# Kernel tuning notes

Hardware: AMD Instinct MI355X
Metric: run time of the kernel (lower is better)

The kernel has to match this reference:

```python
import jax, jax.numpy as jnp
import numpy as np

N = 100000   # nodes
E = 600000   # edges
D = 128      # d_model
R = 200      # num_relations


def setup_inputs() -> dict:
    key = jax.random.key(0)
    ks = jax.random.split(key, 12)
    def nrm(k, shape, scale=0.02):
        return jax.random.normal(k, shape, jnp.float32) * scale
    return dict(
        node_features=jax.random.normal(ks[0], (N, D), jnp.float32),
        edge_index=jax.random.randint(ks[1], (2, E), 0, N),
        edge_type=jax.random.randint(ks[2], (E,), 0, R),
        rel_embed=nrm(ks[3], (R, D)),
        msg_w1=nrm(ks[4], (2 * D, D)), msg_b1=jnp.zeros((D,), jnp.float32),
        msg_w2=nrm(ks[5], (D, D)), msg_b2=jnp.zeros((D,), jnp.float32),
        attn_w1=nrm(ks[6], (2 * D, D)), attn_b1=jnp.zeros((D,), jnp.float32),
        attn_w2=nrm(ks[7], (D, 1)), attn_b2=jnp.zeros((1,), jnp.float32),
        ln1_g=jnp.ones((D,), jnp.float32), ln1_b=jnp.zeros((D,), jnp.float32),
        ffn_w1=nrm(ks[8], (D, 4 * D)), ffn_b1=jnp.zeros((4 * D,), jnp.float32),
        ffn_w2=nrm(ks[9], (4 * D, D)), ffn_b2=jnp.zeros((D,), jnp.float32),
        ln2_g=jnp.ones((D,), jnp.float32), ln2_b=jnp.zeros((D,), jnp.float32),
    )


def layer_norm(x, g, b, eps=1e-5):
    mu = x.mean(-1, keepdims=True)
    var = ((x - mu) ** 2).mean(-1, keepdims=True)
    return (x - mu) * jax.lax.rsqrt(var + eps) * g + b


def reference(node_features, edge_index, edge_type, rel_embed,
              msg_w1, msg_b1, msg_w2, msg_b2,
              attn_w1, attn_b1, attn_w2, attn_b2,
              ln1_g, ln1_b, ffn_w1, ffn_b1, ffn_w2, ffn_b2,
              ln2_g, ln2_b):
    Nn = node_features.shape[0]
    src, dst = edge_index[0], edge_index[1]
    # gather + edge message MLP
    src_feat = node_features[src]              # [E, D]
    rel_feat = rel_embed[edge_type]            # [E, D]
    h = jnp.concatenate([src_feat, rel_feat], axis=-1)          # [E, 2D]
    messages = jax.nn.relu(h @ msg_w1 + msg_b1) @ msg_w2 + msg_b2  # [E, D]
    # edge attention logits
    a_in = jnp.concatenate([node_features[dst], messages], axis=-1)  # [E, 2D]
    attn_raw = (jax.nn.leaky_relu(a_in @ attn_w1 + attn_b1, 0.2) @ attn_w2 + attn_b2)[:, 0]  # [E]
    # two-pass segment softmax over destination nodes
    attn_max = jax.ops.segment_max(attn_raw, dst, num_segments=Nn)   # [N]
    attn_exp = jnp.exp(attn_raw - attn_max[dst])                      # [E]
    attn_sum = jax.ops.segment_sum(attn_exp, dst, num_segments=Nn)   # [N]
    attn_w = attn_exp / (attn_sum[dst] + 1e-8)                        # [E]
    # scatter-add weighted messages
    aggr = jax.ops.segment_sum(attn_w[:, None] * messages, dst, num_segments=Nn)  # [N, D]
    x = layer_norm(node_features + aggr, ln1_g, ln1_b)
    ffn = jax.nn.gelu(x @ ffn_w1 + ffn_b1, approximate=False) @ ffn_w2 + ffn_b2
    return layer_norm(x + ffn, ln2_g, ln2_b)
```

## Files before the change

kernel.cpp:

```cpp
#include <hip/hip_runtime.h>
#include <hip/hip_bf16.h>

#define NN 100000
#define NE 600000
#define DD 128
#define RR 200
#define SCAN_NB ((NN + 255) / 256)

typedef __attribute__((ext_vector_type(8))) short bf16x8;
typedef __attribute__((ext_vector_type(4))) float f32x4;

__device__ __forceinline__ unsigned int bfbits(float x) {
    return (unsigned int)__builtin_bit_cast(unsigned short, __float2bfloat16(x));
}
__device__ __forceinline__ unsigned int pk2(float a, float b) {
    return bfbits(a) | (bfbits(b) << 16);
}
__device__ __forceinline__ unsigned short bf16s(float x) {
    return __builtin_bit_cast(unsigned short, __float2bfloat16(x));
}
__device__ __forceinline__ float unbf(unsigned short u) {
    return __builtin_bit_cast(float, ((unsigned int)u) << 16);
}
__device__ __forceinline__ float unlo(unsigned int u) {
    return __builtin_bit_cast(float, u << 16);
}
__device__ __forceinline__ float unhi(unsigned int u) {
    return __builtin_bit_cast(float, u & 0xffff0000u);
}

__device__ __forceinline__ void gload_lds16(const void* g, void* l) {
    __builtin_amdgcn_global_load_lds(
        (const __attribute__((address_space(1))) void*)g,
        (__attribute__((address_space(3))) void*)l, 16, 0, 0);
}

__global__ void k_initc(int* __restrict__ cnt) {
    int i = blockIdx.x * 256 + threadIdx.x;
    if (i < NN) cnt[i] = 0;
}

__global__ void k_hist(const int* __restrict__ dst, int* __restrict__ cnt) {
    int e = blockIdx.x * 256 + threadIdx.x;
    if (e < NE) atomicAdd(&cnt[dst[e]], 1);
}

__global__ void k_scanA(const int* __restrict__ cnt, int* __restrict__ bsum) {
    __shared__ int red[256];
    int i = blockIdx.x * 256 + threadIdx.x;
    red[threadIdx.x] = (i < NN) ? cnt[i] : 0;
    __syncthreads();
    for (int off = 128; off >= 1; off >>= 1) {
        if (threadIdx.x < off) red[threadIdx.x] += red[threadIdx.x + off];
        __syncthreads();
    }
    if (threadIdx.x == 0) bsum[blockIdx.x] = red[0];
}

__global__ void k_scanB(int* __restrict__ bsum) {
    __shared__ int sh[512];
    int t = threadIdx.x;
    int v = (t < SCAN_NB) ? bsum[t] : 0;
    sh[t] = v;
    __syncthreads();
    for (int off = 1; off < 512; off <<= 1) {
        int add = (t >= off) ? sh[t - off] : 0;
        __syncthreads();
        sh[t] += add;
        __syncthreads();
    }
    if (t < SCAN_NB) bsum[t] = sh[t] - v;
}

__global__ void k_scanC(const int* __restrict__ cnt, const int* __restrict__ bsum,
                        int* __restrict__ row_start, int* __restrict__ cursor) {
    __shared__ int sh[256];
    int i = blockIdx.x * 256 + threadIdx.x;
    int t = threadIdx.x;
    int v = (i < NN) ? cnt[i] : 0;
    sh[t] = v;
    __syncthreads();
    for (int off = 1; off < 256; off <<= 1) {
        int add = (t >= off) ? sh[t - off] : 0;
        __syncthreads();
        sh[t] += add;
        __syncthreads();
    }
    if (i < NN) {
        int ex = bsum[blockIdx.x] + sh[t] - v;
        row_start[i] = ex;
        cursor[i] = ex;
    }
}

__global__ void k_bucket(const int* __restrict__ dst, int* __restrict__ cursor,
                         int* __restrict__ eid) {
    int e = blockIdx.x * 256 + threadIdx.x;
    if (e < NE) {
        int p = atomicAdd(&cursor[dst[e]], 1);
        eid[p] = e;
    }
}

__global__ void k_prep(const float* __restrict__ nf, unsigned short* __restrict__ nfb) {
    int i = blockIdx.x * 256 + threadIdx.x;
    if (i >= NN * DD / 8) return;
    const float* sp = nf + (size_t)i * 8;
    float4 f0 = *reinterpret_cast<const float4*>(sp);
    float4 f1 = *reinterpret_cast<const float4*>(sp + 4);
    uint4 v;
    v.x = pk2(f0.x, f0.y); v.y = pk2(f0.z, f0.w);
    v.z = pk2(f1.x, f1.y); v.w = pk2(f1.z, f1.w);
    *reinterpret_cast<uint4*>(nfb + (size_t)i * 8) = v;
}

__global__ void k_relc(const float* __restrict__ rel, const float* __restrict__ mw1,
                       const float* __restrict__ mb1, unsigned short* __restrict__ relcb) {
    int idx = blockIdx.x * 256 + threadIdx.x;
    if (idx >= RR * DD) return;
    int r = idx >> 7, n = idx & 127;
    float s = mb1[n];
    for (int k = 0; k < 128; ++k)
        s = fmaf(rel[r * 128 + k], mw1[(128 + k) * 128 + n], s);
    relcb[idx] = bf16s(s);
}

__global__ void k_mwb(const float* __restrict__ mw2, const float* __restrict__ mb2,
                      const float* __restrict__ aw1,
                      float* __restrict__ mwB, float* __restrict__ zb) {
    int idx = blockIdx.x * 256 + threadIdx.x;
    if (idx < 16384) {
        int k = idx >> 7, n = idx & 127;
        float s = 0.0f;
        for (int j = 0; j < 128; ++j)
            s = fmaf(mw2[k * 128 + j], aw1[(128 + j) * 128 + n], s);
        mwB[idx] = s;
    } else if (idx < 16512) {
        int n = idx - 16384;
        float s = 0.0f;
        for (int j = 0; j < 128; ++j)
            s = fmaf(mb2[j], aw1[(128 + j) * 128 + n], s);
        zb[n] = s;
    }
}

__global__ void k_pack(const float* __restrict__ mw1, const float* __restrict__ mw2,
                       const float* __restrict__ mwB,
                       const float* __restrict__ aw1,
                       const float* __restrict__ fw1, const float* __restrict__ fw2,
                       unsigned short* __restrict__ mw1p,
                       unsigned short* __restrict__ mwCp,
                       unsigned short* __restrict__ awTp,
                       unsigned short* __restrict__ fw1p,
                       unsigned short* __restrict__ fw2p) {
    int idx = blockIdx.x * 256 + threadIdx.x;
    if (idx < 16384) {
        int i = idx & 7, l = (idx >> 3) & 63, ks = (idx >> 9) & 3, nt = idx >> 11;
        int k = ks * 32 + (l >> 4) * 8 + i, n = nt * 16 + (l & 15);
        mw1p[idx] = bf16s(mw1[k * 128 + n]);
    } else if (idx < 49152) {
        int j = idx - 16384;
        int i = j & 7, l = (j >> 3) & 63, ks = (j >> 9) & 3, nt = j >> 11;
        int k = ks * 32 + (l >> 4) * 8 + i, n = nt * 16 + (l & 15);
        mwCp[j] = bf16s((n < 128) ? mw2[k * 128 + n] : mwB[k * 128 + (n - 128)]);
    } else if (idx < 65536) {
        int j = idx - 49152;
        int i = j & 7, l = (j >> 3) & 63, ks = (j >> 9) & 3, nt = j >> 11;
        int k = ks * 32 + (l >> 4) * 8 + i, n = nt * 16 + (l & 15);
        awTp[j] = bf16s(aw1[k * 128 + n]);
    } else if (idx < 131072) {
        int j = idx - 65536;
        int i = j & 7, l = (j >> 3) & 63, ks = (j >> 9) & 3, nt = j >> 11;
        int k = ks * 32 + (l >> 4) * 8 + i, n = nt * 16 + (l & 15);
        fw1p[j] = bf16s(fw1[k * 512 + n]);
    } else if (idx < 196608) {
        int j = idx - 131072;
        int i = j & 7, l = (j >> 3) & 63, ks = (j >> 9) & 15, nt = j >> 13;
        int k = ks * 32 + (l >> 4) * 8 + i, n = nt * 16 + (l & 15);
        fw2p[j] = bf16s(fw2[k * 128 + n]);
    }
}

__global__ __launch_bounds__(256) void k_nfa(
    const unsigned short* __restrict__ nfb, const unsigned short* __restrict__ awTp,
    const float* __restrict__ ab1, unsigned short* __restrict__ nfa)
{
    __shared__ alignas(16) unsigned short XB[64 * 128];
    const int t = threadIdx.x;
    const int w = t >> 6, l = t & 63;
    const int wm = w >> 1, wn = w & 1;
    const int lm = l & 15, lk = l >> 4;
    const int lrow = l >> 4, lslot = l & 15;
    const int n0 = blockIdx.x * 64;

    #pragma unroll
    for (int it = 0; it < 4; ++it) {
        int rb = w * 16 + it * 4;
        int row = rb + lrow;
        long grow = n0 + row; if (grow >= NN) grow = NN - 1;
        int c = lslot ^ (row & 7);
        gload_lds16(nfb + grow * DD + c * 8, &XB[rb * 128]);
    }
    __syncthreads();

    f32x4 acc[2][4];
    #pragma unroll
    for (int mf = 0; mf < 2; ++mf)
        #pragma unroll
        for (int nfr = 0; nfr < 4; ++nfr) acc[mf][nfr] = (f32x4){0.f, 0.f, 0.f, 0.f};

    #pragma unroll
    for (int ks = 0; ks < 4; ++ks) {
        bf16x8 a[2];
        #pragma unroll
        for (int mf = 0; mf < 2; ++mf) {
            int m = wm * 32 + mf * 16 + lm;
            int slot = (ks * 4 + lk) ^ (m & 7);
            a[mf] = *reinterpret_cast<const bf16x8*>(&XB[m * 128 + slot * 8]);
        }
        #pragma unroll
        for (int nfr = 0; nfr < 4; ++nfr) {
            int nt = wn * 4 + nfr;
            bf16x8 b = *reinterpret_cast<const bf16x8*>(&awTp[((nt * 4 + ks) * 64 + l) * 8]);
            acc[0][nfr] = __builtin_amdgcn_mfma_f32_16x16x32_bf16(a[0], b, acc[0][nfr], 0, 0, 0);
            acc[1][nfr] = __builtin_amdgcn_mfma_f32_16x16x32_bf16(a[1], b, acc[1][nfr], 0, 0, 0);
        }
    }
    __syncthreads();

    #pragma unroll
    for (int nfr = 0; nfr < 4; ++nfr) {
        int n = wn * 64 + nfr * 16 + lm;
        float bv = ab1[n];
        #pragma unroll
        for (int mf = 0; mf < 2; ++mf)
            #pragma unroll
            for (int r = 0; r < 4; ++r) {
                int m = wm * 32 + mf * 16 + lk * 4 + r;
                XB[m * 128 + n] = bf16s(acc[mf][nfr][r] + bv);
            }
    }
    __syncthreads();

    #pragma unroll
    for (int j = 0; j < 4; ++j) {
        int q = j * 256 + t;
        int row = q >> 4, c16 = q & 15;
        if (n0 + row < NN)
            *reinterpret_cast<uint4*>(&nfa[(size_t)(n0 + row) * DD + c16 * 8]) =
                *reinterpret_cast<const uint4*>(&XB[row * 128 + c16 * 8]);
    }
}

__global__ __launch_bounds__(512) void k_edge(
    const unsigned short* __restrict__ nfb, const int* __restrict__ src,
    const int* __restrict__ dst, const int* __restrict__ etype,
    const unsigned short* __restrict__ nfa, const unsigned short* __restrict__ relcb,
    const unsigned short* __restrict__ mw1p, const unsigned short* __restrict__ mwCp,
    const float* __restrict__ mb2, const float* __restrict__ zb,
    const float* __restrict__ aw2, const float* __restrict__ ab2,
    unsigned short* __restrict__ msg_out, float* __restrict__ attn_raw)
{
    __shared__ alignas(16) unsigned short S[64 * 128];
    __shared__ alignas(16) unsigned short H[64 * 128];
    __shared__ alignas(16) unsigned short MS[64 * 128];
    __shared__ float RED[64][2];

    const int t = threadIdx.x;
    const int w = t >> 6, l = t & 63;
    const int wm = w >> 2, wn = w & 3;
    const int lm = l & 15, lk = l >> 4;
    const int lrow = l >> 4, lslot = l & 15;
    const int e0 = blockIdx.x * 64;

    #pragma unroll
    for (int it = 0; it < 2; ++it) {
        int rb = w * 8 + it * 4;
        int row = rb + lrow;
        int c = lslot ^ (row & 7);
        gload_lds16(nfb + (size_t)src[e0 + row] * DD + c * 8, &S[rb * 128]);
    }
    #pragma unroll
    for (int it = 0; it < 2; ++it) {
        int rb = w * 8 + it * 4;
        int row = rb + lrow;
        int c = lslot ^ (row & 7);
        gload_lds16(relcb + (size_t)etype[e0 + row] * DD + c * 8, &MS[rb * 128]);
    }
    __syncthreads();

    {
        f32x4 acc[2][2];
        #pragma unroll
        for (int mf = 0; mf < 2; ++mf)
            #pragma unroll
            for (int nfr = 0; nfr < 2; ++nfr) acc[mf][nfr] = (f32x4){0.f, 0.f, 0.f, 0.f};

        #pragma unroll
        for (int ks = 0; ks < 4; ++ks) {
            bf16x8 a[2];
            #pragma unroll
            for (int mf = 0; mf < 2; ++mf) {
                int m = wm * 32 + mf * 16 + lm;
                int slot = (ks * 4 + lk) ^ (m & 7);
                a[mf] = *reinterpret_cast<const bf16x8*>(&S[m * 128 + slot * 8]);
            }
            #pragma unroll
            for (int nfr = 0; nfr < 2; ++nfr) {
                int nt = wn * 2 + nfr;
                bf16x8 b = *reinterpret_cast<const bf16x8*>(&mw1p[((nt * 4 + ks) * 64 + l) * 8]);
                acc[0][nfr] = __builtin_amdgcn_mfma_f32_16x16x32_bf16(a[0], b, acc[0][nfr], 0, 0, 0);
                acc[1][nfr] = __builtin_amdgcn_mfma_f32_16x16x32_bf16(a[1], b, acc[1][nfr], 0, 0, 0);
            }
        }
        #pragma unroll
        for (int nfr = 0; nfr < 2; ++nfr) {
            int n = (wn * 2 + nfr) * 16 + lm;
            #pragma unroll
            for (int mf = 0; mf < 2; ++mf)
                #pragma unroll
                for (int r = 0; r < 4; ++r) {
                    int m = wm * 32 + mf * 16 + lk * 4 + r;
                    float v = acc[mf][nfr][r] + unbf(MS[m * 128 + ((n >> 3) ^ (m & 7)) * 8 + (n & 7)]);
                    v = fmaxf(v, 0.0f);
                    H[m * 128 + ((n >> 3) ^ (m & 7)) * 8 + (n & 7)] = bf16s(v);
                }
        }
    }
    __syncthreads();

    #pragma unroll
    for (int it = 0; it < 2; ++it) {
        int rb = w * 8 + it * 4;
        int row = rb + lrow;
        int c = lslot ^ (row & 7);
        gload_lds16(nfa + (size_t)dst[e0 + row] * DD + c * 8, &S[rb * 128]);
    }

    f32x4 acc[2][4];
    #pragma unroll
    for (int mf = 0; mf < 2; ++mf)
        #pragma unroll
        for (int nfr = 0; nfr < 4; ++nfr) acc[mf][nfr] = (f32x4){0.f, 0.f, 0.f, 0.f};

    #pragma unroll
    for (int ks = 0; ks < 4; ++ks) {
        bf16x8 a[2];
        #pragma unroll
        for (int mf = 0; mf < 2; ++mf) {
            int m = wm * 32 + mf * 16 + lm;
            int slot = (ks * 4 + lk) ^ (m & 7);
            a[mf] = *reinterpret_cast<const bf16x8*>(&H[m * 128 + slot * 8]);
        }
        #pragma unroll
        for (int nfr = 0; nfr < 4; ++nfr) {
            int nt = wn * 4 + nfr;
            bf16x8 b = *reinterpret_cast<const bf16x8*>(&mwCp[((nt * 4 + ks) * 64 + l) * 8]);
            acc[0][nfr] = __builtin_amdgcn_mfma_f32_16x16x32_bf16(a[0], b, acc[0][nfr], 0, 0, 0);
            acc[1][nfr] = __builtin_amdgcn_mfma_f32_16x16x32_bf16(a[1], b, acc[1][nfr], 0, 0, 0);
        }
    }
    __syncthreads();

    if (wn < 2) {
        #pragma unroll
        for (int nfr = 0; nfr < 4; ++nfr) {
            int n = (wn * 4 + nfr) * 16 + lm;
            float bv = mb2[n];
            #pragma unroll
            for (int mf = 0; mf < 2; ++mf)
                #pragma unroll
                for (int r = 0; r < 4; ++r) {
                    int m = wm * 32 + mf * 16 + lk * 4 + r;
                    MS[m * 128 + ((n >> 3) ^ (m & 7)) * 8 + (n & 7)] = bf16s(acc[mf][nfr][r] + bv);
                }
        }
    } else {
        float zbv[4], aw2v[4];
        #pragma unroll
        for (int nfr = 0; nfr < 4; ++nfr) {
            int nc = (wn - 2) * 64 + nfr * 16 + lm;
            zbv[nfr] = zb[nc];
            aw2v[nfr] = aw2[nc];
        }
        #pragma unroll
        for (int mf = 0; mf < 2; ++mf)
            #pragma unroll
            for (int r = 0; r < 4; ++r) {
                int m = wm * 32 + mf * 16 + lk * 4 + r;
                float s = 0.0f;
                #pragma unroll
                for (int nfr = 0; nfr < 4; ++nfr) {
                    int nc = (wn - 2) * 64 + nfr * 16 + lm;
                    float v = acc[mf][nfr][r] + zbv[nfr]
                            + unbf(S[m * 128 + ((nc >> 3) ^ (m & 7)) * 8 + (nc & 7)]);
                    v = (v > 0.0f) ? v : 0.2f * v;
                    s = fmaf(v, aw2v[nfr], s);
                }
                s += __shfl_xor(s, 1, 64);
                s += __shfl_xor(s, 2, 64);
                s += __shfl_xor(s, 4, 64);
                s += __shfl_xor(s, 8, 64);
                if (lm == 0) RED[m][wn - 2] = s;
            }
    }
    __syncthreads();

    #pragma unroll
    for (int j = 0; j < 2; ++j) {
        int q = j * 512 + t;
        int row = q >> 4, c16 = q & 15;
        int slot = c16 ^ (row & 7);
        *reinterpret_cast<uint4*>(&msg_out[(size_t)(e0 + row) * DD + c16 * 8]) =
            *reinterpret_cast<const uint4*>(&MS[row * 128 + slot * 8]);
    }
    if (t < 64) {
        attn_raw[e0 + t] = RED[t][0] + RED[t][1] + ab2[0];
    }
}

__global__ __launch_bounds__(256) void k_aggr(
    const unsigned short* __restrict__ msg, const float* __restrict__ raw,
    const int* __restrict__ row_start, const int* __restrict__ cnt,
    const int* __restrict__ eid, float* __restrict__ aggr)
{
    const int l = threadIdx.x & 63;
    const int n = blockIdx.x * 4 + (threadIdx.x >> 6);
    if (n >= NN) return;
    const int rs = row_start[n], deg = cnt[n];

    float m = -INFINITY;
    for (int j = l; j < deg; j += 64) m = fmaxf(m, raw[eid[rs + j]]);
    #pragma unroll
    for (int off = 32; off >= 1; off >>= 1) m = fmaxf(m, __shfl_xor(m, off, 64));

    float s = 0.0f;
    for (int j = l; j < deg; j += 64) s += expf(raw[eid[rs + j]] - m);
    #pragma unroll
    for (int off = 32; off >= 1; off >>= 1) s += __shfl_xor(s, off, 64);
    const float rinv = 1.0f / (s + 1e-8f);

    float a0 = 0.0f, a1 = 0.0f;
    for (int base = 0; base < deg; base += 64) {
        int nt = min(64, deg - base);
        int e_l = 0; float w_l = 0.0f;
        if (l < nt) {
            e_l = eid[rs + base + l];
            w_l = expf(raw[e_l] - m) * rinv;
        }
        for (int j = 0; j < nt; ++j) {
            int e = __shfl(e_l, j, 64);
            float w = __shfl(w_l, j, 64);
            unsigned int v = *reinterpret_cast<const unsigned int*>(&msg[(size_t)e * DD + l * 2]);
            a0 = fmaf(w, unlo(v), a0);
            a1 = fmaf(w, unhi(v), a1);
        }
    }
    float2 o = {a0, a1};
    *reinterpret_cast<float2*>(&aggr[(size_t)n * DD + l * 2]) = o;
}

__global__ __launch_bounds__(512) void k_node(
    const float* __restrict__ nf, const float* __restrict__ aggr,
    const float* __restrict__ g1, const float* __restrict__ b1,
    const unsigned short* __restrict__ fw1p, const float* __restrict__ fb1,
    const unsigned short* __restrict__ fw2p, const float* __restrict__ fb2,
    const float* __restrict__ g2, const float* __restrict__ b2,
    float* __restrict__ out)
{
    __shared__ alignas(16) unsigned short XB[64 * 128];
    __shared__ alignas(16) unsigned short HB[64 * 256];

    const int t = threadIdx.x;
    const int w = t >> 6, l = t & 63;
    const int wm = w >> 2, wn = w & 3;
    const int lm = l & 15, lk = l >> 4;
    const int row = t >> 3;
    const int q = t & 7;
    const long n0 = (long)blockIdx.x * 64;
    const long rg = n0 + row;
    const long rc = (rg < NN) ? rg : (NN - 1);

    float xr[16];
    float s = 0.0f, ss = 0.0f;
    {
        const float* xp = nf + rc * DD + q * 16;
        const float* ap = aggr + rc * DD + q * 16;
        #pragma unroll
        for (int i = 0; i < 4; ++i) {
            float4 a = *reinterpret_cast<const float4*>(xp + i * 4);
            float4 b = *reinterpret_cast<const float4*>(ap + i * 4);
            float v0 = a.x + b.x, v1 = a.y + b.y, v2 = a.z + b.z, v3 = a.w + b.w;
            xr[i * 4 + 0] = v0; xr[i * 4 + 1] = v1; xr[i * 4 + 2] = v2; xr[i * 4 + 3] = v3;
            s += v0 + v1 + v2 + v3;
            ss = fmaf(v0, v0, ss); ss = fmaf(v1, v1, ss);
            ss = fmaf(v2, v2, ss); ss = fmaf(v3, v3, ss);
        }
    }
    s  += __shfl_xor(s, 1, 64);  s  += __shfl_xor(s, 2, 64);  s  += __shfl_xor(s, 4, 64);
    ss += __shfl_xor(ss, 1, 64); ss += __shfl_xor(ss, 2, 64); ss += __shfl_xor(ss, 4, 64);
    {
        float mu = s * (1.0f / DD);
        float var = ss * (1.0f / DD) - mu * mu;
        float rstd = rsqrtf(var + 1e-5f);
        #pragma unroll
        for (int i = 0; i < 4; ++i) {
            float4 gv = *reinterpret_cast<const float4*>(g1 + q * 16 + i * 4);
            float4 bv = *reinterpret_cast<const float4*>(b1 + q * 16 + i * 4);
            xr[i * 4 + 0] = (xr[i * 4 + 0] - mu) * rstd * gv.x + bv.x;
            xr[i * 4 + 1] = (xr[i * 4 + 1] - mu) * rstd * gv.y + bv.y;
            xr[i * 4 + 2] = (xr[i * 4 + 2] - mu) * rstd * gv.z + bv.z;
            xr[i * 4 + 3] = (xr[i * 4 + 3] - mu) * rstd * gv.w + bv.w;
        }
        #pragma unroll
        for (int i = 0; i < 2; ++i) {
            int c = q * 2 + i, slot = c ^ (row & 7);
            uint4 v;
            v.x = pk2(xr[i * 8 + 0], xr[i * 8 + 1]);
            v.y = pk2(xr[i * 8 + 2], xr[i * 8 + 3]);
            v.z = pk2(xr[i * 8 + 4], xr[i * 8 + 5]);
            v.w = pk2(xr[i * 8 + 6], xr[i * 8 + 7]);
            *reinterpret_cast<uint4*>(&XB[row * 128 + slot * 8]) = v;
        }
    }
    __syncthreads();

    f32x4 acc2[2][2];
    #pragma unroll
    for (int mf = 0; mf < 2; ++mf)
        #pragma unroll
        for (int nfr = 0; nfr < 2; ++nfr) acc2[mf][nfr] = (f32x4){0.f, 0.f, 0.f, 0.f};

    #pragma unroll
    for (int half = 0; half < 2; ++half) {
        f32x4 acc[2][4];
        #pragma unroll
        for (int mf = 0; mf < 2; ++mf)
            #pragma unroll
            for (int nfr = 0; nfr < 4; ++nfr) acc[mf][nfr] = (f32x4){0.f, 0.f, 0.f, 0.f};

        #pragma unroll
        for (int ks = 0; ks < 4; ++ks) {
            bf16x8 a[2];
            #pragma unroll
            for (int mf = 0; mf < 2; ++mf) {
                int m = wm * 32 + mf * 16 + lm;
                int slot = (ks * 4 + lk) ^ (m & 7);
                a[mf] = *reinterpret_cast<const bf16x8*>(&XB[m * 128 + slot * 8]);
            }
            #pragma unroll
            for (int nfr = 0; nfr < 4; ++nfr) {
                int nt = half * 16 + wn * 4 + nfr;
                bf16x8 b = *reinterpret_cast<const bf16x8*>(&fw1p[((nt * 4 + ks) * 64 + l) * 8]);
                acc[0][nfr] = __builtin_amdgcn_mfma_f32_16x16x32_bf16(a[0], b, acc[0][nfr], 0, 0, 0);
                acc[1][nfr] = __builtin_amdgcn_mfma_f32_16x16x32_bf16(a[1], b, acc[1][nfr], 0, 0, 0);
            }
        }
        #pragma unroll
        for (int nfr = 0; nfr < 4; ++nfr) {
            int nl = (wn * 4 + nfr) * 16 + lm;
            float bv = fb1[half * 256 + nl];
            #pragma unroll
            for (int mf = 0; mf < 2; ++mf)
                #pragma unroll
                for (int r = 0; r < 4; ++r) {
                    int m = wm * 32 + mf * 16 + lk * 4 + r;
                    float h = acc[mf][nfr][r] + bv;
                    float e = __expf(h * -1.702f);
                    float gvv = h * __builtin_amdgcn_rcpf(1.0f + e);
                    HB[m * 256 + (((nl >> 3) ^ (m & 7)) * 8) + (nl & 7)] = bf16s(gvv);
                }
        }
        __syncthreads();

        #pragma unroll
        for (int ks = 0; ks < 8; ++ks) {
            bf16x8 a[2];
            #pragma unroll
            for (int mf = 0; mf < 2; ++mf) {
                int m = wm * 32 + mf * 16 + lm;
                int slot = (ks * 4 + lk) ^ (m & 7);
                a[mf] = *reinterpret_cast<const bf16x8*>(&HB[m * 256 + slot * 8]);
            }
            #pragma unroll
            for (int nfr = 0; nfr < 2; ++nfr) {
                int nt = wn * 2 + nfr;
                int kg = half * 8 + ks;
                bf16x8 b = *reinterpret_cast<const bf16x8*>(&fw2p[((nt * 16 + kg) * 64 + l) * 8]);
                acc2[0][nfr] = __builtin_amdgcn_mfma_f32_16x16x32_bf16(a[0], b, acc2[0][nfr], 0, 0, 0);
                acc2[1][nfr] = __builtin_amdgcn_mfma_f32_16x16x32_bf16(a[1], b, acc2[1][nfr], 0, 0, 0);
            }
        }
        __syncthreads();
    }

    #pragma unroll
    for (int nfr = 0; nfr < 2; ++nfr) {
        int n = (wn * 2 + nfr) * 16 + lm;
        float bv = fb2[n];
        #pragma unroll
        for (int mf = 0; mf < 2; ++mf)
            #pragma unroll
            for (int r = 0; r < 4; ++r) {
                int m = wm * 32 + mf * 16 + lk * 4 + r;
                XB[m * 128 + (((n >> 3) ^ (m & 7)) * 8) + (n & 7)] = bf16s(acc2[mf][nfr][r] + bv);
            }
    }
    __syncthreads();

    float s2 = 0.0f, ss2 = 0.0f;
    #pragma unroll
    for (int i = 0; i < 2; ++i) {
        int c = q * 2 + i, slot = c ^ (row & 7);
        uint4 v = *reinterpret_cast<const uint4*>(&XB[row * 128 + slot * 8]);
        float f[8];
        f[0] = unlo(v.x); f[1] = unhi(v.x); f[2] = unlo(v.y); f[3] = unhi(v.y);
        f[4] = unlo(v.z); f[5] = unhi(v.z); f[6] = unlo(v.w); f[7] = unhi(v.w);
        #pragma unroll
        for (int j = 0; j < 8; ++j) {
            float vv = xr[i * 8 + j] + f[j];
            xr[i * 8 + j] = vv;
            s2 += vv;
            ss2 = fmaf(vv, vv, ss2);
        }
    }
    s2  += __shfl_xor(s2, 1, 64);  s2  += __shfl_xor(s2, 2, 64);  s2  += __shfl_xor(s2, 4, 64);
    ss2 += __shfl_xor(ss2, 1, 64); ss2 += __shfl_xor(ss2, 2, 64); ss2 += __shfl_xor(ss2, 4, 64);
    {
        float mu = s2 * (1.0f / DD);
        float var = ss2 * (1.0f / DD) - mu * mu;
        float rstd = rsqrtf(var + 1e-5f);
        if (rg < NN) {
            float* op = out + rg * DD + q * 16;
            #pragma unroll
            for (int i = 0; i < 4; ++i) {
                float4 gv = *reinterpret_cast<const float4*>(g2 + q * 16 + i * 4);
                float4 bv = *reinterpret_cast<const float4*>(b2 + q * 16 + i * 4);
                float4 o;
                o.x = (xr[i * 4 + 0] - mu) * rstd * gv.x + bv.x;
                o.y = (xr[i * 4 + 1] - mu) * rstd * gv.y + bv.y;
                o.z = (xr[i * 4 + 2] - mu) * rstd * gv.z + bv.z;
                o.w = (xr[i * 4 + 3] - mu) * rstd * gv.w + bv.w;
                *reinterpret_cast<float4*>(op + i * 4) = o;
            }
        }
    }
}

extern "C" void kernel_launch(void* const* d_in, const int* in_sizes, int n_in,
                              void* d_out, int out_size, void* d_ws, size_t ws_size,
                              hipStream_t stream)
{
    const float* nf  = (const float*)d_in[0];
    const int*   ei  = (const int*)d_in[1];
    const int*   et  = (const int*)d_in[2];
    const float* rel = (const float*)d_in[3];
    const float* mw1 = (const float*)d_in[4];
    const float* mb1 = (const float*)d_in[5];
    const float* mw2 = (const float*)d_in[6];
    const float* mb2 = (const float*)d_in[7];
    const float* aw1 = (const float*)d_in[8];
    const float* ab1 = (const float*)d_in[9];
    const float* aw2 = (const float*)d_in[10];
    const float* ab2 = (const float*)d_in[11];
    const float* g1  = (const float*)d_in[12];
    const float* b1  = (const float*)d_in[13];
    const float* fw1 = (const float*)d_in[14];
    const float* fb1 = (const float*)d_in[15];
    const float* fw2 = (const float*)d_in[16];
    const float* fb2 = (const float*)d_in[17];
    const float* g2  = (const float*)d_in[18];
    const float* b2  = (const float*)d_in[19];
    float* out = (float*)d_out;

    char* ws = (char*)d_ws;
    size_t off = 0;
    auto alloc = [&](size_t bytes) -> char* {
        char* p = ws + off;
        off += (bytes + 255) & ~(size_t)255;
        return p;
    };
    unsigned short* msg = (unsigned short*)alloc((size_t)NE * DD * 2);
    float* attn_raw = (float*)alloc((size_t)NE * 4);
    float* aggr     = (float*)alloc((size_t)NN * DD * 4);
    unsigned short* nfb  = (unsigned short*)alloc((size_t)NN * DD * 2);
    unsigned short* relcb = (unsigned short*)alloc((size_t)RR * DD * 2);
    float* mwB = (float*)alloc((size_t)16384 * 4);
    float* zb  = (float*)alloc((size_t)128 * 4);
    int* cnt       = (int*)alloc((size_t)NN * 4);
    int* row_start = (int*)alloc((size_t)NN * 4);
    int* cursor    = (int*)alloc((size_t)NN * 4);
    int* eid       = (int*)alloc((size_t)NE * 4);
    int* bsum      = (int*)alloc((size_t)SCAN_NB * 4);
    unsigned short* mw1p = (unsigned short*)alloc(16384 * 2);
    unsigned short* mwCp = (unsigned short*)alloc(32768 * 2);
    unsigned short* awTp = (unsigned short*)alloc(16384 * 2);
    unsigned short* fw1p = (unsigned short*)alloc(65536 * 2);
    unsigned short* fw2p = (unsigned short*)alloc(65536 * 2);

    unsigned short* nfa = (unsigned short*)aggr;

    const int* srcp = ei;
    const int* dstp = ei + NE;

    hipLaunchKernelGGL(k_initc, dim3(SCAN_NB), dim3(256), 0, stream, cnt);
    hipLaunchKernelGGL(k_hist, dim3((NE + 255) / 256), dim3(256), 0, stream, dstp, cnt);
    hipLaunchKernelGGL(k_scanA, dim3(SCAN_NB), dim3(256), 0, stream, cnt, bsum);
    hipLaunchKernelGGL(k_scanB, dim3(1), dim3(512), 0, stream, bsum);
    hipLaunchKernelGGL(k_scanC, dim3(SCAN_NB), dim3(256), 0, stream, cnt, bsum, row_start, cursor);
    hipLaunchKernelGGL(k_bucket, dim3((NE + 255) / 256), dim3(256), 0, stream, dstp, cursor, eid);
    hipLaunchKernelGGL(k_prep, dim3(NN * DD / 8 / 256), dim3(256), 0, stream, nf, nfb);
    hipLaunchKernelGGL(k_mwb, dim3(65), dim3(256), 0, stream, mw2, mb2, aw1, mwB, zb);
    hipLaunchKernelGGL(k_pack, dim3(768), dim3(256), 0, stream,
                       mw1, mw2, mwB, aw1, fw1, fw2, mw1p, mwCp, awTp, fw1p, fw2p);
    hipLaunchKernelGGL(k_relc, dim3(100), dim3(256), 0, stream, rel, mw1, mb1, relcb);
    hipLaunchKernelGGL(k_nfa, dim3((NN + 63) / 64), dim3(256), 0, stream,
                       nfb, awTp, ab1, nfa);
    hipLaunchKernelGGL(k_edge, dim3(NE / 64), dim3(512), 0, stream,
                       nfb, srcp, dstp, et, nfa, relcb,
                       mw1p, mwCp, mb2, zb, aw2, ab2,
                       msg, attn_raw);
    hipLaunchKernelGGL(k_aggr, dim3((NN + 3) / 4), dim3(256), 0, stream,
                       msg, attn_raw, row_start, cnt, eid, aggr);
    hipLaunchKernelGGL(k_node, dim3((NN + 63) / 64), dim3(512), 0, stream,
                       nf, aggr, g1, b1, fw1p, fb1, fw2p, fb2, g2, b2, out);
}
```

Measured before the change: 482.2 us.

## Process edges in destination-sorted order so aggregation reads contiguous messages

Result: faster. 471.6 us (-2.2%).

```diff
diff --git a/kernel.cpp b/kernel.cpp
--- a/kernel.cpp
+++ b/kernel.cpp
@@ -93,12 +93,17 @@
     }
 }
 
-__global__ void k_bucket(const int* __restrict__ dst, int* __restrict__ cursor,
-                         int* __restrict__ eid) {
+__global__ void k_bucket(const int* __restrict__ src, const int* __restrict__ dst,
+                         const int* __restrict__ etype, int* __restrict__ cursor,
+                         int* __restrict__ srcs, int* __restrict__ ets,
+                         int* __restrict__ dsts) {
     int e = blockIdx.x * 256 + threadIdx.x;
     if (e < NE) {
-        int p = atomicAdd(&cursor[dst[e]], 1);
-        eid[p] = e;
+        int d = dst[e];
+        int p = atomicAdd(&cursor[d], 1);
+        srcs[p] = src[e];
+        ets[p]  = etype[e];
+        dsts[p] = d;
     }
 }
 
@@ -253,8 +258,8 @@
 }
 
 __global__ __launch_bounds__(512) void k_edge(
-    const unsigned short* __restrict__ nfb, const int* __restrict__ src,
-    const int* __restrict__ dst, const int* __restrict__ etype,
+    const unsigned short* __restrict__ nfb, const int* __restrict__ srcs,
+    const int* __restrict__ dsts, const int* __restrict__ ets,
     const unsigned short* __restrict__ nfa, const unsigned short* __restrict__ relcb,
     const unsigned short* __restrict__ mw1p, const unsigned short* __restrict__ mwCp,
     const float* __restrict__ mb2, const float* __restrict__ zb,
@@ -263,7 +268,6 @@
 {
     __shared__ alignas(16) unsigned short S[64 * 128];
     __shared__ alignas(16) unsigned short H[64 * 128];
-    __shared__ alignas(16) unsigned short MS[64 * 128];
     __shared__ float RED[64][2];
 
     const int t = threadIdx.x;
@@ -278,14 +282,14 @@
         int rb = w * 8 + it * 4;
         int row = rb + lrow;
         int c = lslot ^ (row & 7);
-        gload_lds16(nfb + (size_t)src[e0 + row] * DD + c * 8, &S[rb * 128]);
+        gload_lds16(nfb + (size_t)srcs[e0 + row] * DD + c * 8, &S[rb * 128]);
     }
     #pragma unroll
     for (int it = 0; it < 2; ++it) {
         int rb = w * 8 + it * 4;
         int row = rb + lrow;
         int c = lslot ^ (row & 7);
-        gload_lds16(relcb + (size_t)etype[e0 + row] * DD + c * 8, &MS[rb * 128]);
+        gload_lds16(relcb + (size_t)ets[e0 + row] * DD + c * 8, &H[rb * 128]);
     }
     __syncthreads();
 
@@ -321,9 +325,10 @@
                 #pragma unroll
                 for (int r = 0; r < 4; ++r) {
                     int m = wm * 32 + mf * 16 + lk * 4 + r;
-                    float v = acc[mf][nfr][r] + unbf(MS[m * 128 + ((n >> 3) ^ (m & 7)) * 8 + (n & 7)]);
+                    int sl = m * 128 + ((n >> 3) ^ (m & 7)) * 8 + (n & 7);
+                    float v = acc[mf][nfr][r] + unbf(H[sl]);
                     v = fmaxf(v, 0.0f);
-                    H[m * 128 + ((n >> 3) ^ (m & 7)) * 8 + (n & 7)] = bf16s(v);
+                    H[sl] = bf16s(v);
                 }
         }
     }
@@ -334,7 +339,7 @@
         int rb = w * 8 + it * 4;
         int row = rb + lrow;
         int c = lslot ^ (row & 7);
-        gload_lds16(nfa + (size_t)dst[e0 + row] * DD + c * 8, &S[rb * 128]);
+        gload_lds16(nfa + (size_t)dsts[e0 + row] * DD + c * 8, &S[rb * 128]);
     }
 
     f32x4 acc[2][4];
@@ -372,7 +377,7 @@
                 #pragma unroll
                 for (int r = 0; r < 4; ++r) {
                     int m = wm * 32 + mf * 16 + lk * 4 + r;
-                    MS[m * 128 + ((n >> 3) ^ (m & 7)) * 8 + (n & 7)] = bf16s(acc[mf][nfr][r] + bv);
+                    H[m * 128 + ((n >> 3) ^ (m & 7)) * 8 + (n & 7)] = bf16s(acc[mf][nfr][r] + bv);
                 }
         }
     } else {
@@ -412,7 +417,7 @@
         int row = q >> 4, c16 = q & 15;
         int slot = c16 ^ (row & 7);
         *reinterpret_cast<uint4*>(&msg_out[(size_t)(e0 + row) * DD + c16 * 8]) =
-            *reinterpret_cast<const uint4*>(&MS[row * 128 + slot * 8]);
+            *reinterpret_cast<const uint4*>(&H[row * 128 + slot * 8]);
     }
     if (t < 64) {
         attn_raw[e0 + t] = RED[t][0] + RED[t][1] + ab2[0];
@@ -422,7 +427,7 @@
 __global__ __launch_bounds__(256) void k_aggr(
     const unsigned short* __restrict__ msg, const float* __restrict__ raw,
     const int* __restrict__ row_start, const int* __restrict__ cnt,
-    const int* __restrict__ eid, float* __restrict__ aggr)
+    float* __restrict__ aggr)
 {
     const int l = threadIdx.x & 63;
     const int n = blockIdx.x * 4 + (threadIdx.x >> 6);
@@ -430,31 +435,23 @@
     const int rs = row_start[n], deg = cnt[n];
 
     float m = -INFINITY;
-    for (int j = l; j < deg; j += 64) m = fmaxf(m, raw[eid[rs + j]]);
+    for (int j = l; j < deg; j += 64) m = fmaxf(m, raw[rs + j]);
     #pragma unroll
     for (int off = 32; off >= 1; off >>= 1) m = fmaxf(m, __shfl_xor(m, off, 64));
 
     float s = 0.0f;
-    for (int j = l; j < deg; j += 64) s += expf(raw[eid[rs + j]] - m);
+    for (int j = l; j < deg; j += 64) s += expf(raw[rs + j] - m);
     #pragma unroll
     for (int off = 32; off >= 1; off >>= 1) s += __shfl_xor(s, off, 64);
     const float rinv = 1.0f / (s + 1e-8f);
 
     float a0 = 0.0f, a1 = 0.0f;
-    for (int base = 0; base < deg; base += 64) {
-        int nt = min(64, deg - base);
-        int e_l = 0; float w_l = 0.0f;
-        if (l < nt) {
-            e_l = eid[rs + base + l];
-            w_l = expf(raw[e_l] - m) * rinv;
-        }
-        for (int j = 0; j < nt; ++j) {
-            int e = __shfl(e_l, j, 64);
-            float w = __shfl(w_l, j, 64);
-            unsigned int v = *reinterpret_cast<const unsigned int*>(&msg[(size_t)e * DD + l * 2]);
-            a0 = fmaf(w, unlo(v), a0);
-            a1 = fmaf(w, unhi(v), a1);
-        }
+    for (int j = 0; j < deg; ++j) {
+        float w = expf(raw[rs + j] - m) * rinv;
+        unsigned int v = *reinterpret_cast<const unsigned int*>(
+            &msg[(size_t)(rs + j) * DD + l * 2]);
+        a0 = fmaf(w, unlo(v), a0);
+        a1 = fmaf(w, unhi(v), a1);
     }
     float2 o = {a0, a1};
     *reinterpret_cast<float2*>(&aggr[(size_t)n * DD + l * 2]) = o;
@@ -690,7 +687,9 @@
     int* cnt       = (int*)alloc((size_t)NN * 4);
     int* row_start = (int*)alloc((size_t)NN * 4);
     int* cursor    = (int*)alloc((size_t)NN * 4);
-    int* eid       = (int*)alloc((size_t)NE * 4);
+    int* srcs      = (int*)alloc((size_t)NE * 4);
+    int* ets       = (int*)alloc((size_t)NE * 4);
+    int* dsts      = (int*)alloc((size_t)NE * 4);
     int* bsum      = (int*)alloc((size_t)SCAN_NB * 4);
     unsigned short* mw1p = (unsigned short*)alloc(16384 * 2);
     unsigned short* mwCp = (unsigned short*)alloc(32768 * 2);
@@ -708,7 +707,8 @@
     hipLaunchKernelGGL(k_scanA, dim3(SCAN_NB), dim3(256), 0, stream, cnt, bsum);
     hipLaunchKernelGGL(k_scanB, dim3(1), dim3(512), 0, stream, bsum);
     hipLaunchKernelGGL(k_scanC, dim3(SCAN_NB), dim3(256), 0, stream, cnt, bsum, row_start, cursor);
-    hipLaunchKernelGGL(k_bucket, dim3((NE + 255) / 256), dim3(256), 0, stream, dstp, cursor, eid);
+    hipLaunchKernelGGL(k_bucket, dim3((NE + 255) / 256), dim3(256), 0, stream,
+                       srcp, dstp, et, cursor, srcs, ets, dsts);
     hipLaunchKernelGGL(k_prep, dim3(NN * DD / 8 / 256), dim3(256), 0, stream, nf, nfb);
     hipLaunchKernelGGL(k_mwb, dim3(65), dim3(256), 0, stream, mw2, mb2, aw1, mwB, zb);
     hipLaunchKernelGGL(k_pack, dim3(768), dim3(256), 0, stream,
@@ -717,11 +717,11 @@
     hipLaunchKernelGGL(k_nfa, dim3((NN + 63) / 64), dim3(256), 0, stream,
                        nfb, awTp, ab1, nfa);
     hipLaunchKernelGGL(k_edge, dim3(NE / 64), dim3(512), 0, stream,
-                       nfb, srcp, dstp, et, nfa, relcb,
+                       nfb, srcs, dsts, ets, nfa, relcb,
                        mw1p, mwCp, mb2, zb, aw2, ab2,
                        msg, attn_raw);
     hipLaunchKernelGGL(k_aggr, dim3((NN + 3) / 4), dim3(256), 0, stream,
-                       msg, attn_raw, row_start, cnt, eid, aggr);
+                       msg, attn_raw, row_start, cnt, aggr);
     hipLaunchKernelGGL(k_node, dim3((NN + 63) / 64), dim3(512), 0, stream,
                        nf, aggr, g1, b1, fw1p, fb1, fw2p, fb2, g2, b2, out);
 }
```
